# Kernel tuning notes

Measured on AMD Instinct MI355X. Metric: run time of the kernel, lower is better.

Reference implementation:

```python
import jax, jax.numpy as jnp
import numpy as np

N = 50000        # atoms
E = 1600000      # edges (precomputed radius graph)
H = 128          # hidden_channels
F = 64           # num_filters
G = 50           # num_gaussians
L = 3            # num_interactions
NG = 256         # graphs in batch
MAXZ = 100       # atomic-number vocabulary
CUTOFF = 10.0


def ssp(x):
    # ShiftedSoftplus
    return jax.nn.softplus(x) - jnp.log(2.0).astype(x.dtype)


def setup_inputs() -> dict:
    key = jax.random.key(0)
    ks = jax.random.split(key, 20)
    s = 0.1
    inp = {
        "z": jax.random.randint(ks[0], (N,), 0, MAXZ),
        "pos": jax.random.uniform(ks[1], (N, 3), dtype=jnp.float32) * 5.0,
        "batch": jnp.sort(jax.random.randint(ks[2], (N,), 0, NG)),
        "edge_index": jax.random.randint(ks[3], (2, E), 0, N),
        "emb": jax.random.normal(ks[4], (MAXZ, H), dtype=jnp.float32),
        # interaction-block params, stacked over L layers
        "mw1": jax.random.normal(ks[5], (L, G, F), dtype=jnp.float32) * s,
        "mb1": jnp.zeros((L, F), dtype=jnp.float32),
        "mw2": jax.random.normal(ks[6], (L, F, F), dtype=jnp.float32) * s,
        "mb2": jnp.zeros((L, F), dtype=jnp.float32),
        "l1w": jax.random.normal(ks[7], (L, H, F), dtype=jnp.float32) * s,  # no bias
        "l2w": jax.random.normal(ks[8], (L, F, H), dtype=jnp.float32) * s,
        "l2b": jnp.zeros((L, H), dtype=jnp.float32),
        "lw": jax.random.normal(ks[9], (L, H, H), dtype=jnp.float32) * s,
        "lb": jnp.zeros((L, H), dtype=jnp.float32),
        # output MLP
        "ow1": jax.random.normal(ks[10], (H, H // 2), dtype=jnp.float32) * s,
        "ob1": jnp.zeros((H // 2,), dtype=jnp.float32),
        "ow2": jax.random.normal(ks[11], (H // 2, 1), dtype=jnp.float32) * s,
        "ob2": jnp.zeros((1,), dtype=jnp.float32),
    }
    return inp


def reference(z, pos, batch, edge_index, emb, mw1, mb1, mw2, mb2,
              l1w, l2w, l2b, lw, lb, ow1, ob1, ow2, ob2):
    src = edge_index[0]  # j (message source)
    dst = edge_index[1]  # i (message target)

    h = emb[z]                                   # [N,H]

    # edge distances + Gaussian smearing
    d = jnp.linalg.norm(pos[src] - pos[dst], axis=-1)          # [E]
    offset = jnp.linspace(0.0, CUTOFF, G, dtype=jnp.float32)   # [G]
    coeff = -0.5 / (offset[1] - offset[0]) ** 2
    edge_attr = jnp.exp(coeff * (d[:, None] - offset) ** 2)    # [E,G]

    # cosine cutoff
    C = 0.5 * (jnp.cos(d * jnp.pi / CUTOFF) + 1.0)             # [E]

    for i in range(L):
        # per-edge filter MLP
        W = ssp(edge_attr @ mw1[i] + mb1[i]) @ mw2[i] + mb2[i]  # [E,F]
        W = W * C[:, None]
        xj = (h @ l1w[i])[src]                                  # gather [E,F]
        msg = xj * W                                            # [E,F]
        agg = jax.ops.segment_sum(msg, dst, num_segments=N)     # [N,F]
        x = agg @ l2w[i] + l2b[i]                               # [N,H]
        x = ssp(x)
        x = x @ lw[i] + lb[i]
        h = h + x                                               # residual

    # output network + per-graph sum readout
    h = ssp(h @ ow1 + ob1)
    h = h @ ow2 + ob2                                           # [N,1]
    out = jax.ops.segment_sum(h, batch, num_segments=NG)        # [NG,1]
    return out.squeeze(1)                                       # [NG]
```

## Files before the change

kernel.cpp:

```cpp
#include <hip/hip_runtime.h>


typedef short bf16x8 __attribute__((ext_vector_type(8)));
typedef unsigned short ushort8 __attribute__((ext_vector_type(8)));
typedef float floatx4 __attribute__((ext_vector_type(4)));

#define HCH 128
#define FCH 64
#define GCH 50
#define LN  3
#define TBL 4096
#define CAP1 6144
#define CHUNK 2048
#define DMAX 8.6603f

#define MFMA(a, b, c) __builtin_amdgcn_mfma_f32_16x16x32_bf16((a), (b), (c), 0, 0, 0)

__device__ __forceinline__ unsigned short f2bf(float x) {
    unsigned int u = __float_as_uint(x);
    unsigned int r = (u + 0x7FFFu + ((u >> 16) & 1u)) >> 16;
    return (unsigned short)r;
}

__device__ __forceinline__ unsigned pk2bf(float lo, float hi) {
    unsigned ulo = __float_as_uint(lo) + 0x8000u;
    unsigned uhi = __float_as_uint(hi) + 0x8000u;
    return __builtin_amdgcn_perm(uhi, ulo, 0x07060302u);
}

__device__ __forceinline__ float bf2f(unsigned short u) {
    return __uint_as_float((unsigned)u << 16);
}

__device__ __forceinline__ float sspf(float x) {
    float t = __expf(-fabsf(x));
    float l = __logf(1.f + t);
    return fmaxf(x, 0.f) + l - 0.69314718056f;
}

__device__ __forceinline__ void fill_frag(const float* __restrict__ src,
                                          short* __restrict__ dst,
                                          int K, int F, int Ksrc,
                                          int tid, int nthr)
{
    int kc = K >> 5;
    int total = (F >> 4) * kc * 512;
    for (int i = tid; i < total; i += nthr) {
        int j = i & 7;
        int lane = (i >> 3) & 63;
        int rest = i >> 9;
        int kk = rest % kc;
        int nt = rest / kc;
        int k = kk * 32 + ((lane >> 4) << 3) + j;
        int f = nt * 16 + (lane & 15);
        float v = (k < Ksrc) ? src[k * F + f] : 0.f;
        dst[i] = (short)f2bf(v);
    }
}

__global__ void k_prep(const float* __restrict__ l1w, const float* __restrict__ l2w,
                       const float* __restrict__ lw,  const float* __restrict__ ow1,
                       short* __restrict__ l1wp, short* __restrict__ l2wp,
                       short* __restrict__ lwp,  short* __restrict__ ow1p)
{
    int tid = blockIdx.x * blockDim.x + threadIdx.x;
    int nthr = gridDim.x * blockDim.x;
    for (int l = 0; l < LN; l++) {
        fill_frag(l1w + l * HCH * FCH, l1wp + l * 8192, 128, 64, 128, tid, nthr);
        fill_frag(l2w + l * FCH * HCH, l2wp + l * 8192, 64, 128, 64, tid, nthr);
        fill_frag(lw  + l * HCH * HCH, lwp  + l * 16384, 128, 128, 128, tid, nthr);
    }
    fill_frag(ow1, ow1p, 128, 64, 128, tid, nthr);
}

__global__ __launch_bounds__(64) void k_wtab(
    const float* __restrict__ mw1, const float* __restrict__ mb1,
    const float* __restrict__ mw2, const float* __restrict__ mb2,
    unsigned short* __restrict__ Wtb)
{
    __shared__ float sh[64];
    int blk = blockIdx.x;
    int l = blk / TBL, k = blk - l * TBL;
    int f = threadIdx.x;
    float d = (float)k * (DMAX / (float)(TBL - 1));
    const float step = 10.f / 49.f;
    const float coeff = -0.5f / (step * step);

    float t1 = mb1[l * 64 + f];
    const float* w1 = mw1 + l * GCH * 64;
    for (int g = 0; g < GCH; g++) {
        float u = d - (float)g * step;
        t1 += __expf(coeff * u * u) * w1[g * 64 + f];
    }
    sh[f] = sspf(t1);
    float acc = mb2[l * 64 + f];
    const float* w2 = mw2 + l * 64 * 64;
    for (int g = 0; g < 64; g++) acc += sh[g] * w2[g * 64 + f];
    float C = 0.5f * (__cosf(d * 0.31415926535897932f) + 1.f);
    Wtb[(size_t)blk * 64 + f] = f2bf(acc * C);
}

__global__ __launch_bounds__(256, 4) void k_s1(
    const int* __restrict__ ei, const float* __restrict__ pos,
    int* __restrict__ gcur, int2* __restrict__ ebuf, int E, int nb1)
{
    __shared__ int hist[512];
    __shared__ int lstart[512];
    __shared__ int lcur[512];
    __shared__ int gbase[512];
    __shared__ int wsum[4];
    __shared__ int2 stage[CHUNK];

    int t = threadIdx.x, lane = t & 63, w = t >> 6;
    int e0 = blockIdx.x * CHUNK;
    int e1 = min(e0 + CHUNK, E);
    int cnt = e1 - e0;

    for (int i = t; i < 512; i += 256) hist[i] = 0;
    __syncthreads();

    int esrc[8], edst[8];
    float psx[8], psy[8], psz[8], pdx[8], pdy[8], pdz[8];
#pragma unroll
    for (int i = 0; i < 8; i++) {
        int e = e0 + t + i * 256;
        bool v = e < e1;
        int s = 0, d2 = 0;
        if (v) { s = ei[e]; d2 = ei[E + e]; }
        esrc[i] = s;
        edst[i] = v ? d2 : -1;
        if (v) {
            psx[i] = pos[s * 3 + 0]; psy[i] = pos[s * 3 + 1]; psz[i] = pos[s * 3 + 2];
            pdx[i] = pos[d2 * 3 + 0]; pdy[i] = pos[d2 * 3 + 1]; pdz[i] = pos[d2 * 3 + 2];
        }
    }
    int2 my[8];
    int  mybk[8];
#pragma unroll
    for (int i = 0; i < 8; i++) {
        if (edst[i] >= 0) {
            float dx = psx[i] - pdx[i];
            float dy = psy[i] - pdy[i];
            float dz = psz[i] - pdz[i];
            float dist = sqrtf(dx * dx + dy * dy + dz * dz);
            int tix = (int)(dist * ((float)(TBL - 1) / DMAX) + 0.5f);
            tix = (tix > TBL - 1) ? (TBL - 1) : tix;
            int bk = edst[i] >> 7;
            my[i] = make_int2(esrc[i] | (tix << 17), edst[i]);
            mybk[i] = bk;
            atomicAdd(&hist[bk], 1);
        } else {
            mybk[i] = -1;
        }
    }
    __syncthreads();

    {
        int base = w * 128;
        int c0 = hist[base + lane];
        int c1 = hist[base + 64 + lane];
        int a = c0, b = c1;
#pragma unroll
        for (int o = 1; o < 64; o <<= 1) {
            int ua = __shfl_up(a, o, 64);
            int ub = __shfl_up(b, o, 64);
            if (lane >= o) { a += ua; b += ub; }
        }
        int atot = __shfl(a, 63, 64);
        b += atot;
        if (lane == 63) wsum[w] = b;
        __syncthreads();
        int prefix = 0;
#pragma unroll
        for (int i = 0; i < 4; i++) if (i < w) prefix += wsum[i];
        int ls0 = prefix + a - c0;
        int ls1 = prefix + b - c1;
        int bk0 = base + lane, bk1 = base + 64 + lane;
        lstart[bk0] = ls0; lcur[bk0] = ls0;
        lstart[bk1] = ls1; lcur[bk1] = ls1;
        int base0 = (c0 && bk0 < nb1) ? atomicAdd(&gcur[bk0 * 16], c0) : 0;
        int base1 = (c1 && bk1 < nb1) ? atomicAdd(&gcur[bk1 * 16], c1) : 0;
        gbase[bk0] = bk0 * CAP1 + base0;
        gbase[bk1] = bk1 * CAP1 + base1;
    }
    __syncthreads();

#pragma unroll
    for (int i = 0; i < 8; i++) {
        if (mybk[i] >= 0) {
            int ofs = atomicAdd(&lcur[mybk[i]], 1);
            stage[ofs] = my[i];
        }
    }
    __syncthreads();

    for (int i = t; i < cnt; i += 256) {
        int2 ed = stage[i];
        int bk = ed.y >> 7;
        int g = gbase[bk] + (i - lstart[bk]);
        if (g < bk * CAP1 + CAP1) ebuf[g] = ed;
    }
}

__global__ __launch_bounds__(512) void k_scanB(const int* __restrict__ gcur,
                                               int* __restrict__ bstart, int nb1)
{
    __shared__ int sh[512];
    int t = threadIdx.x;
    int v = (t < nb1) ? min(gcur[t * 16], CAP1) : 0;
    sh[t] = v;
    __syncthreads();
    for (int o = 1; o < 512; o <<= 1) {
        int u = (t >= o) ? sh[t - o] : 0;
        __syncthreads();
        sh[t] += u;
        __syncthreads();
    }
    bstart[t] = sh[t] - v;
}

__global__ __launch_bounds__(512) void k_s2(
    const int2* __restrict__ ebuf, const int* __restrict__ gcur,
    const int* __restrict__ bstart, int2* __restrict__ edata)
{
    __shared__ int hist[128];
    __shared__ int bcur[128];
    int t = threadIdx.x, bk = blockIdx.x;
    int cnt = min(gcur[bk * 16], CAP1);
    int gs = bstart[bk];
    if (t < 128) hist[t] = 0;
    __syncthreads();
    const int2* eb = ebuf + (size_t)bk * CAP1;
    for (int i = t; i < cnt; i += 512)
        atomicAdd(&hist[eb[i].y & 127], 1);
    __syncthreads();
    int myc = (t < 128) ? hist[t] : 0;
    for (int o = 1; o < 128; o <<= 1) {
        int u = (t < 128 && t >= o) ? hist[t - o] : 0;
        __syncthreads();
        if (t < 128) hist[t] += u;
        __syncthreads();
    }
    if (t < 128) bcur[t] = gs + hist[t] - myc;
    __syncthreads();
    for (int i = t; i < cnt; i += 512) {
        int2 ed = eb[i];
        int dl = ed.y & 127;
        int p = atomicAdd(&bcur[dl], 1);
        edata[p] = ed;
    }
}

__global__ __launch_bounds__(256) void k_node0(const int* __restrict__ z,
    const float* __restrict__ emb, const short* __restrict__ l1wp0,
    float* __restrict__ h, unsigned short* __restrict__ xjb,
    float* __restrict__ agg, int N)
{
    __shared__ __align__(16) short A3[8192];
    __shared__ int zL[64];
    int t = threadIdx.x, lane = t & 63, w = t >> 6;
    int n0 = blockIdx.x * 64;
    if (t < 64) { int n = n0 + t; zL[t] = (n < N) ? z[n] : 0; }
    __syncthreads();
    for (int i = t; i < 4096; i += 256) {
        int n = n0 + (i >> 6);
        if (n < N) agg[(size_t)n * FCH + (i & 63)] = 0.f;
    }
#pragma unroll
    for (int m = 0; m < 16; m++) {
        int ii = lane + 64 * m;
        int rloc = ii >> 6;
        int k0 = (ii & 63) * 2;
        int n = n0 + w * 16 + rloc;
        float2 v = make_float2(0.f, 0.f);
        if (n < N) {
            v = *(const float2*)(&emb[(size_t)zL[w * 16 + rloc] * HCH + k0]);
            *(float2*)(&h[(size_t)n * HCH + k0]) = v;
        }
        unsigned pk = pk2bf(v.x, v.y);
        int si = w * 2048 + (k0 >> 5) * 512 + (rloc + 16 * ((k0 >> 3) & 3)) * 8 + (k0 & 7);
        *(unsigned*)(&A3[si]) = pk;
    }
    int quad = lane >> 4, col = lane & 15;
    const bf16x8* B = (const bf16x8*)l1wp0;
    bf16x8 af[4];
#pragma unroll
    for (int kk = 0; kk < 4; kk++)
        af[kk] = *(const bf16x8*)(&A3[w * 2048 + kk * 512 + lane * 8]);
#pragma unroll
    for (int nt = 0; nt < 4; nt++) {
        floatx4 c = {0.f, 0.f, 0.f, 0.f};
#pragma unroll
        for (int kk = 0; kk < 4; kk++) c = MFMA(af[kk], B[(nt * 4 + kk) * 64 + lane], c);
        int f = nt * 16 + col;
#pragma unroll
        for (int reg = 0; reg < 4; reg++) {
            int n = n0 + w * 16 + quad * 4 + reg;
            if (n < N) xjb[(size_t)n * FCH + f] = f2bf(c[reg]);
        }
    }
}

__global__ __launch_bounds__(256) void k_edge(
    const int2* __restrict__ edata, const unsigned short* __restrict__ xjb,
    const unsigned short* __restrict__ Wt, float* __restrict__ agg, int E)
{
    __shared__ float M[64 * 68];
    __shared__ int tD[64];

    int t = threadIdx.x, lane = t & 63, w = t >> 6;
    int r  = w * 16 + (lane >> 2);
    int fq = lane & 3;
    int eg = blockIdx.x * 64 + r;

    int2 ed = make_int2(0, -1);
    if (eg < E) ed = edata[eg];
    int src = ed.x & 0x1FFFF;
    int tix = ((unsigned)ed.x) >> 17;
    if (fq == 0) tD[r] = ed.y;

    const ushort8* Wr = (const ushort8*)(Wt + ((size_t)tix << 6) + fq * 16);
    const ushort8* X  = (const ushort8*)(xjb + ((size_t)src << 6) + fq * 16);
    ushort8 w0 = Wr[0];
    ushort8 w1 = Wr[1];
    ushort8 xA = X[0];
    ushort8 xB = X[1];

    float* Mr = &M[r * 68 + fq * 16];
    float4 m;
    m.x = bf2f(w0[0]) * bf2f(xA[0]); m.y = bf2f(w0[1]) * bf2f(xA[1]);
    m.z = bf2f(w0[2]) * bf2f(xA[2]); m.w = bf2f(w0[3]) * bf2f(xA[3]);
    *(float4*)(Mr + 0) = m;
    m.x = bf2f(w0[4]) * bf2f(xA[4]); m.y = bf2f(w0[5]) * bf2f(xA[5]);
    m.z = bf2f(w0[6]) * bf2f(xA[6]); m.w = bf2f(w0[7]) * bf2f(xA[7]);
    *(float4*)(Mr + 4) = m;
    m.x = bf2f(w1[0]) * bf2f(xB[0]); m.y = bf2f(w1[1]) * bf2f(xB[1]);
    m.z = bf2f(w1[2]) * bf2f(xB[2]); m.w = bf2f(w1[3]) * bf2f(xB[3]);
    *(float4*)(Mr + 8) = m;
    m.x = bf2f(w1[4]) * bf2f(xB[4]); m.y = bf2f(w1[5]) * bf2f(xB[5]);
    m.z = bf2f(w1[6]) * bf2f(xB[6]); m.w = bf2f(w1[7]) * bf2f(xB[7]);
    *(float4*)(Mr + 12) = m;

    {
        int f = lane;
        int base = w * 16;
        float a = 0.f;
        int cur = tD[base];
#pragma unroll
        for (int i = 0; i < 16; i++) {
            int d2 = tD[base + i];
            if (d2 != cur) {
                if (cur >= 0) unsafeAtomicAdd(&agg[(size_t)cur * FCH + f], a);
                a = 0.f; cur = d2;
            }
            a += M[(base + i) * 68 + f];
        }
        if (cur >= 0) unsafeAtomicAdd(&agg[(size_t)cur * FCH + f], a);
    }
}

__global__ __launch_bounds__(256) void k_update(
    float* __restrict__ agg, const short* __restrict__ l2wp,
    const float* __restrict__ l2b, const short* __restrict__ lwp,
    const float* __restrict__ lb,  const short* __restrict__ l1wp_next,
    float* __restrict__ h, unsigned short* __restrict__ xjb, int layer, int N)
{
    __shared__ __align__(16) short AR[8192];
    int t = threadIdx.x, lane = t & 63, w = t >> 6;
    int n0 = blockIdx.x * 64;
    short* WR = &AR[w * 2048];
#pragma unroll
    for (int m = 0; m < 8; m++) {
        int ii = lane + 64 * m;
        int rloc = ii >> 5;
        int k0 = (ii & 31) * 2;
        int n = n0 + w * 16 + rloc;
        float2 v = make_float2(0.f, 0.f);
        if (n < N) v = *(const float2*)(&agg[(size_t)n * FCH + k0]);
        unsigned pk = pk2bf(v.x, v.y);
        int si = (k0 >> 5) * 512 + (rloc + 16 * ((k0 >> 3) & 3)) * 8 + (k0 & 7);
        *(unsigned*)(&WR[si]) = pk;
    }
#pragma unroll
    for (int i = 0; i < 16; i++) {
        int n = n0 + w * 16 + i;
        if (n < N) agg[(size_t)n * FCH + lane] = 0.f;
    }
    int quad = lane >> 4, col = lane & 15;
    const bf16x8* Bl2 = (const bf16x8*)(l2wp + layer * 8192);
    const bf16x8* Blw = (const bf16x8*)(lwp + layer * 16384);
    const bf16x8* Bl1 = (const bf16x8*)l1wp_next;

    bf16x8 a0 = *(const bf16x8*)(&WR[lane * 8]);
    bf16x8 a1 = *(const bf16x8*)(&WR[512 + lane * 8]);
#pragma unroll
    for (int nt = 0; nt < 8; nt++) {
        float bias = l2b[layer * HCH + nt * 16 + col];
        floatx4 c = {bias, bias, bias, bias};
        c = MFMA(a0, Bl2[(nt * 2 + 0) * 64 + lane], c);
        c = MFMA(a1, Bl2[(nt * 2 + 1) * 64 + lane], c);
        int f = nt * 16 + col;
        int si0 = (f >> 5) * 512 + (16 * ((f >> 3) & 3)) * 8 + (f & 7);
#pragma unroll
        for (int reg = 0; reg < 4; reg++)
            WR[si0 + (quad * 4 + reg) * 8] = (short)f2bf(sspf(c[reg]));
    }
    bf16x8 af[4];
#pragma unroll
    for (int kk = 0; kk < 4; kk++)
        af[kk] = *(const bf16x8*)(&WR[kk * 512 + lane * 8]);
#pragma unroll
    for (int nt = 0; nt < 8; nt++) {
        float bias = lb[layer * HCH + nt * 16 + col];
        floatx4 c = {bias, bias, bias, bias};
#pragma unroll
        for (int kk = 0; kk < 4; kk++) c = MFMA(af[kk], Blw[(nt * 4 + kk) * 64 + lane], c);
        int f = nt * 16 + col;
        int si0 = (f >> 5) * 512 + (16 * ((f >> 3) & 3)) * 8 + (f & 7);
#pragma unroll
        for (int reg = 0; reg < 4; reg++) {
            int n = n0 + w * 16 + quad * 4 + reg;
            float hv = 0.f;
            if (n < N) {
                hv = h[(size_t)n * HCH + f] + c[reg];
                h[(size_t)n * HCH + f] = hv;
            }
            WR[si0 + (quad * 4 + reg) * 8] = (short)f2bf(hv);
        }
    }
#pragma unroll
    for (int kk = 0; kk < 4; kk++)
        af[kk] = *(const bf16x8*)(&WR[kk * 512 + lane * 8]);
#pragma unroll
    for (int nt = 0; nt < 4; nt++) {
        floatx4 c = {0.f, 0.f, 0.f, 0.f};
#pragma unroll
        for (int kk = 0; kk < 4; kk++) c = MFMA(af[kk], Bl1[(nt * 4 + kk) * 64 + lane], c);
        int f = nt * 16 + col;
#pragma unroll
        for (int reg = 0; reg < 4; reg++) {
            int n = n0 + w * 16 + quad * 4 + reg;
            if (n < N) xjb[(size_t)n * FCH + f] = f2bf(c[reg]);
        }
    }
}

__global__ __launch_bounds__(256) void k_final(
    const float* __restrict__ agg, const short* __restrict__ l2wp,
    const float* __restrict__ l2b, const short* __restrict__ lwp,
    const float* __restrict__ lb,  const short* __restrict__ ow1p,
    const float* __restrict__ ob1, const float* __restrict__ ow2,
    const float* __restrict__ ob2, const int* __restrict__ batch,
    const float* __restrict__ h, float* __restrict__ out, int layer, int N)
{
    __shared__ __align__(16) short AR[8192];
    __shared__ float R[64 * 17];
    int t = threadIdx.x, lane = t & 63, w = t >> 6;
    int n0 = blockIdx.x * 64;
    short* WR = &AR[w * 2048];
#pragma unroll
    for (int m = 0; m < 8; m++) {
        int ii = lane + 64 * m;
        int rloc = ii >> 5;
        int k0 = (ii & 31) * 2;
        int n = n0 + w * 16 + rloc;
        float2 v = make_float2(0.f, 0.f);
        if (n < N) v = *(const float2*)(&agg[(size_t)n * FCH + k0]);
        unsigned pk = pk2bf(v.x, v.y);
        int si = (k0 >> 5) * 512 + (rloc + 16 * ((k0 >> 3) & 3)) * 8 + (k0 & 7);
        *(unsigned*)(&WR[si]) = pk;
    }
    int quad = lane >> 4, col = lane & 15;
    const bf16x8* Bl2 = (const bf16x8*)(l2wp + layer * 8192);
    const bf16x8* Blw = (const bf16x8*)(lwp + layer * 16384);
    const bf16x8* Bow = (const bf16x8*)ow1p;

    bf16x8 a0 = *(const bf16x8*)(&WR[lane * 8]);
    bf16x8 a1 = *(const bf16x8*)(&WR[512 + lane * 8]);
#pragma unroll
    for (int nt = 0; nt < 8; nt++) {
        float bias = l2b[layer * HCH + nt * 16 + col];
        floatx4 c = {bias, bias, bias, bias};
        c = MFMA(a0, Bl2[(nt * 2 + 0) * 64 + lane], c);
        c = MFMA(a1, Bl2[(nt * 2 + 1) * 64 + lane], c);
        int f = nt * 16 + col;
        int si0 = (f >> 5) * 512 + (16 * ((f >> 3) & 3)) * 8 + (f & 7);
#pragma unroll
        for (int reg = 0; reg < 4; reg++)
            WR[si0 + (quad * 4 + reg) * 8] = (short)f2bf(sspf(c[reg]));
    }
    bf16x8 af[4];
#pragma unroll
    for (int kk = 0; kk < 4; kk++)
        af[kk] = *(const bf16x8*)(&WR[kk * 512 + lane * 8]);
#pragma unroll
    for (int nt = 0; nt < 8; nt++) {
        float bias = lb[layer * HCH + nt * 16 + col];
        floatx4 c = {bias, bias, bias, bias};
#pragma unroll
        for (int kk = 0; kk < 4; kk++) c = MFMA(af[kk], Blw[(nt * 4 + kk) * 64 + lane], c);
        int f = nt * 16 + col;
        int si0 = (f >> 5) * 512 + (16 * ((f >> 3) & 3)) * 8 + (f & 7);
#pragma unroll
        for (int reg = 0; reg < 4; reg++) {
            int n = n0 + w * 16 + quad * 4 + reg;
            float hv = 0.f;
            if (n < N) hv = h[(size_t)n * HCH + f] + c[reg];
            WR[si0 + (quad * 4 + reg) * 8] = (short)f2bf(hv);
        }
    }
#pragma unroll
    for (int kk = 0; kk < 4; kk++)
        af[kk] = *(const bf16x8*)(&WR[kk * 512 + lane * 8]);
    float p[4] = {0.f, 0.f, 0.f, 0.f};
#pragma unroll
    for (int nt = 0; nt < 4; nt++) {
        float bias = ob1[nt * 16 + col];
        floatx4 c = {bias, bias, bias, bias};
#pragma unroll
        for (int kk = 0; kk < 4; kk++) c = MFMA(af[kk], Bow[(nt * 4 + kk) * 64 + lane], c);
        float w2 = ow2[nt * 16 + col];
#pragma unroll
        for (int reg = 0; reg < 4; reg++) p[reg] += sspf(c[reg]) * w2;
    }
#pragma unroll
    for (int reg = 0; reg < 4; reg++)
        R[(w * 16 + quad * 4 + reg) * 17 + col] = p[reg];
    __syncthreads();
    if (t < 64) {
        int n = n0 + t;
        float v = 0.f;
        int g = -1;
        if (n < N) {
            v = ob2[0];
#pragma unroll
            for (int c2 = 0; c2 < 16; c2++) v += R[t * 17 + c2];
            g = batch[n];
        }
#pragma unroll
        for (int off2 = 1; off2 < 64; off2 <<= 1) {
            float vv = __shfl_down(v, off2, 64);
            int gg = __shfl_down(g, off2, 64);
            if (lane + off2 < 64 && gg == g) v += vv;
        }
        int gp = __shfl_up(g, 1, 64);
        bool head = (lane == 0) || (g != gp);
        if (head && g >= 0) unsafeAtomicAdd(&out[g], v);
    }
}

extern "C" void kernel_launch(void* const* d_in, const int* in_sizes, int n_in,
                              void* d_out, int out_size, void* d_ws, size_t ws_size,
                              hipStream_t stream)
{
    const int*   z    = (const int*)d_in[0];
    const float* pos  = (const float*)d_in[1];
    const int*   batc = (const int*)d_in[2];
    const int*   ei   = (const int*)d_in[3];
    const float* emb  = (const float*)d_in[4];
    const float* mw1  = (const float*)d_in[5];
    const float* mb1  = (const float*)d_in[6];
    const float* mw2  = (const float*)d_in[7];
    const float* mb2  = (const float*)d_in[8];
    const float* l1w  = (const float*)d_in[9];
    const float* l2w  = (const float*)d_in[10];
    const float* l2b  = (const float*)d_in[11];
    const float* lw   = (const float*)d_in[12];
    const float* lb   = (const float*)d_in[13];
    const float* ow1  = (const float*)d_in[14];
    const float* ob1  = (const float*)d_in[15];
    const float* ow2  = (const float*)d_in[16];
    const float* ob2  = (const float*)d_in[17];
    float* out = (float*)d_out;

    int N = in_sizes[0];
    int E = in_sizes[3] / 2;
    int nb1 = (N + 127) >> 7;

    char* ws = (char*)d_ws;
    size_t off = 0;
    auto alloc = [&](size_t bytes) {
        void* p = ws + off;
        off = (off + bytes + 255) & ~(size_t)255;
        return p;
    };
    float* h      = (float*)alloc((size_t)N * HCH * 4);
    unsigned short* xjb = (unsigned short*)alloc((size_t)N * FCH * 2);
    float* agg    = (float*)alloc((size_t)N * FCH * 4);
    int2*  ebuf   = (int2*)alloc((size_t)nb1 * CAP1 * 8);
    int2*  edata  = (int2*)alloc((size_t)E * 8);
    unsigned short* Wtab = (unsigned short*)alloc((size_t)LN * TBL * 64 * 2);
    int*   gcur   = (int*)alloc((size_t)nb1 * 64);
    int*   bstart = (int*)alloc(512 * 4);
    short* l1wp   = (short*)alloc(LN * 8192 * 2);
    short* l2wp   = (short*)alloc(LN * 8192 * 2);
    short* lwp    = (short*)alloc(LN * 16384 * 2);
    short* ow1p   = (short*)alloc(8192 * 2);

    int NB = (N + 63) / 64;
    int EB = (E + 63) / 64;
    int S1B = (E + CHUNK - 1) / CHUNK;

    k_prep<<<32, 256, 0, stream>>>(l1w, l2w, lw, ow1, l1wp, l2wp, lwp, ow1p);
    k_wtab<<<LN * TBL, 64, 0, stream>>>(mw1, mb1, mw2, mb2, Wtab);
    hipMemsetAsync(gcur, 0, (size_t)nb1 * 64, stream);
    k_s1<<<S1B, 256, 0, stream>>>(ei, pos, gcur, ebuf, E, nb1);
    k_scanB<<<1, 512, 0, stream>>>(gcur, bstart, nb1);
    k_s2<<<nb1, 512, 0, stream>>>(ebuf, gcur, bstart, edata);
    hipMemsetAsync(out, 0, (size_t)out_size * sizeof(float), stream);

    k_node0<<<NB, 256, 0, stream>>>(z, emb, l1wp, h, xjb, agg, N);
    for (int l = 0; l < LN; l++) {
        k_edge<<<EB, 256, 0, stream>>>(edata, xjb,
                                       Wtab + (size_t)l * TBL * 64, agg, E);
        if (l < LN - 1) {
            k_update<<<NB, 256, 0, stream>>>(agg, l2wp, l2b, lwp, lb,
                                             l1wp + (l + 1) * 8192, h, xjb, l, N);
        } else {
            k_final<<<NB, 256, 0, stream>>>(agg, l2wp, l2b, lwp, lb, ow1p,
                                            ob1, ow2, ob2, batc, h, out, l, N);
        }
    }
}
```

Baseline: 388.3 us.

## Fold bucket prefix scan into sort pass and shrink binning chunk size

Removes the single-block k_scanB launch. Each k_s2 block now computes its own bucket start offset with a wave-shuffle reduction over the preceding bucket counts, which drops one kernel launch and its serialization. k_s1 now bins 1024 edges per block with 4 edges per thread instead of 8, so more blocks run. It also restructures the loads: edge indices are fetched unconditionally with clamping, and all position gathers are issued before any compute. The launch_bounds occupancy hint is lowered to 2, and twice as many blocks now contend on the global bucket atomics.

```diff
diff --git a/kernel.cpp b/kernel.cpp
--- a/kernel.cpp
+++ b/kernel.cpp
@@ -11,7 +11,7 @@
 #define LN  3
 #define TBL 4096
 #define CAP1 6144
-#define CHUNK 2048
+#define CHUNK 1024
 #define DMAX 8.6603f
 
 #define MFMA(a, b, c) __builtin_amdgcn_mfma_f32_16x16x32_bf16((a), (b), (c), 0, 0, 0)
@@ -100,7 +100,7 @@
     Wtb[(size_t)blk * 64 + f] = f2bf(acc * C);
 }
 
-__global__ __launch_bounds__(256, 4) void k_s1(
+__global__ __launch_bounds__(256, 2) void k_s1(
     const int* __restrict__ ei, const float* __restrict__ pos,
     int* __restrict__ gcur, int2* __restrict__ ebuf, int E, int nb1)
 {
@@ -119,39 +119,36 @@
     for (int i = t; i < 512; i += 256) hist[i] = 0;
     __syncthreads();
 
-    int esrc[8], edst[8];
-    float psx[8], psy[8], psz[8], pdx[8], pdy[8], pdz[8];
-#pragma unroll
-    for (int i = 0; i < 8; i++) {
+    int esrc[4], edst[4];
+    float psx[4], psy[4], psz[4], pdx[4], pdy[4], pdz[4];
+    bool val[4];
+#pragma unroll
+    for (int i = 0; i < 4; i++) {
         int e = e0 + t + i * 256;
-        bool v = e < e1;
-        int s = 0, d2 = 0;
-        if (v) { s = ei[e]; d2 = ei[E + e]; }
-        esrc[i] = s;
-        edst[i] = v ? d2 : -1;
-        if (v) {
-            psx[i] = pos[s * 3 + 0]; psy[i] = pos[s * 3 + 1]; psz[i] = pos[s * 3 + 2];
-            pdx[i] = pos[d2 * 3 + 0]; pdy[i] = pos[d2 * 3 + 1]; pdz[i] = pos[d2 * 3 + 2];
-        }
-    }
-    int2 my[8];
-    int  mybk[8];
-#pragma unroll
-    for (int i = 0; i < 8; i++) {
-        if (edst[i] >= 0) {
-            float dx = psx[i] - pdx[i];
-            float dy = psy[i] - pdy[i];
-            float dz = psz[i] - pdz[i];
-            float dist = sqrtf(dx * dx + dy * dy + dz * dz);
-            int tix = (int)(dist * ((float)(TBL - 1) / DMAX) + 0.5f);
-            tix = (tix > TBL - 1) ? (TBL - 1) : tix;
-            int bk = edst[i] >> 7;
-            my[i] = make_int2(esrc[i] | (tix << 17), edst[i]);
-            mybk[i] = bk;
-            atomicAdd(&hist[bk], 1);
-        } else {
-            mybk[i] = -1;
-        }
+        val[i] = e < e1;
+        int ec = min(e, E - 1);
+        esrc[i] = ei[ec];
+        edst[i] = ei[E + ec];
+    }
+#pragma unroll
+    for (int i = 0; i < 4; i++) {
+        int s = esrc[i], d2 = edst[i];
+        psx[i] = pos[s * 3 + 0]; psy[i] = pos[s * 3 + 1]; psz[i] = pos[s * 3 + 2];
+        pdx[i] = pos[d2 * 3 + 0]; pdy[i] = pos[d2 * 3 + 1]; pdz[i] = pos[d2 * 3 + 2];
+    }
+    int2 my[4];
+    int  mybk[4];
+#pragma unroll
+    for (int i = 0; i < 4; i++) {
+        float dx = psx[i] - pdx[i];
+        float dy = psy[i] - pdy[i];
+        float dz = psz[i] - pdz[i];
+        float dist = sqrtf(dx * dx + dy * dy + dz * dz);
+        int tix = (int)(dist * ((float)(TBL - 1) / DMAX) + 0.5f);
+        tix = (tix > TBL - 1) ? (TBL - 1) : tix;
+        my[i] = make_int2(esrc[i] | (tix << 17), edst[i]);
+        mybk[i] = val[i] ? (edst[i] >> 7) : -1;
+        if (mybk[i] >= 0) atomicAdd(&hist[mybk[i]], 1);
     }
     __syncthreads();
 
@@ -186,7 +183,7 @@
     __syncthreads();
 
 #pragma unroll
-    for (int i = 0; i < 8; i++) {
+    for (int i = 0; i < 4; i++) {
         if (mybk[i] >= 0) {
             int ofs = atomicAdd(&lcur[mybk[i]], 1);
             stage[ofs] = my[i];
@@ -202,34 +199,26 @@
     }
 }
 
-__global__ __launch_bounds__(512) void k_scanB(const int* __restrict__ gcur,
-                                               int* __restrict__ bstart, int nb1)
-{
-    __shared__ int sh[512];
-    int t = threadIdx.x;
-    int v = (t < nb1) ? min(gcur[t * 16], CAP1) : 0;
-    sh[t] = v;
-    __syncthreads();
-    for (int o = 1; o < 512; o <<= 1) {
-        int u = (t >= o) ? sh[t - o] : 0;
-        __syncthreads();
-        sh[t] += u;
-        __syncthreads();
-    }
-    bstart[t] = sh[t] - v;
-}
-
 __global__ __launch_bounds__(512) void k_s2(
     const int2* __restrict__ ebuf, const int* __restrict__ gcur,
-    const int* __restrict__ bstart, int2* __restrict__ edata)
+    int2* __restrict__ edata, int nb1)
 {
     __shared__ int hist[128];
     __shared__ int bcur[128];
-    int t = threadIdx.x, bk = blockIdx.x;
+    __shared__ int wred[8];
+    int t = threadIdx.x, lane = t & 63, w = t >> 6, bk = blockIdx.x;
     int cnt = min(gcur[bk * 16], CAP1);
-    int gs = bstart[bk];
+
+    int v = (t < bk && t < nb1) ? min(gcur[t * 16], CAP1) : 0;
+#pragma unroll
+    for (int o = 32; o; o >>= 1) v += __shfl_down(v, o, 64);
+    if (lane == 0) wred[w] = v;
     if (t < 128) hist[t] = 0;
     __syncthreads();
+    int gs = 0;
+#pragma unroll
+    for (int i = 0; i < 8; i++) gs += wred[i];
+
     const int2* eb = ebuf + (size_t)bk * CAP1;
     for (int i = t; i < cnt; i += 512)
         atomicAdd(&hist[eb[i].y & 127], 1);
@@ -591,7 +580,6 @@
     int2*  edata  = (int2*)alloc((size_t)E * 8);
     unsigned short* Wtab = (unsigned short*)alloc((size_t)LN * TBL * 64 * 2);
     int*   gcur   = (int*)alloc((size_t)nb1 * 64);
-    int*   bstart = (int*)alloc(512 * 4);
     short* l1wp   = (short*)alloc(LN * 8192 * 2);
     short* l2wp   = (short*)alloc(LN * 8192 * 2);
     short* lwp    = (short*)alloc(LN * 16384 * 2);
@@ -605,8 +593,7 @@
     k_wtab<<<LN * TBL, 64, 0, stream>>>(mw1, mb1, mw2, mb2, Wtab);
     hipMemsetAsync(gcur, 0, (size_t)nb1 * 64, stream);
     k_s1<<<S1B, 256, 0, stream>>>(ei, pos, gcur, ebuf, E, nb1);
-    k_scanB<<<1, 512, 0, stream>>>(gcur, bstart, nb1);
-    k_s2<<<nb1, 512, 0, stream>>>(ebuf, gcur, bstart, edata);
+    k_s2<<<nb1, 512, 0, stream>>>(ebuf, gcur, edata, nb1);
     hipMemsetAsync(out, 0, (size_t)out_size * sizeof(float), stream);
 
     k_node0<<<NB, 256, 0, stream>>>(z, emb, l1wp, h, xjb, agg, N);
```

Measured after the change: 383.8 us, median of 2. No clear change (-1.2%).
